# Performance work log

Hardware: AMD Instinct MI355X
Metric: run time of the kernel (lower is better)

## Reference

```python
import jax, jax.numpy as jnp
import numpy as np

N_NODES, N_EDGES = 8, 8
NODE_FEAT, EDGE_FEAT = 4, 3
NODE_EMB, EDGE_EMB = 9, 8
N_LAYER = 3
N_QUBITS = NODE_EMB + EDGE_EMB + 2  # 19

H_GATE = (jnp.array([[1, 1], [1, -1]], jnp.complex64) / np.sqrt(2).astype(np.float32))
CNOT4 = jnp.asarray(np.array([[1, 0, 0, 0], [0, 1, 0, 0], [0, 0, 0, 1], [0, 0, 1, 0]],
                             np.complex64).reshape(2, 2, 2, 2))


def rx_mat(t):
    c = jnp.cos(0.5 * t).astype(jnp.complex64)
    s = (-1j) * jnp.sin(0.5 * t).astype(jnp.complex64)
    return jnp.stack([jnp.stack([c, s]), jnp.stack([s, c])])


def rz_mat(t):
    e = jnp.exp(-0.5j * t.astype(jnp.complex64))
    z = jnp.zeros((), jnp.complex64)
    return jnp.stack([jnp.stack([e, z]), jnp.stack([z, jnp.conj(e)])])


def apply_1q(psi, U, w):
    psi = jnp.tensordot(U, psi, axes=((1,), (w,)))
    return jnp.moveaxis(psi, 0, w)


def apply_cnot(psi, c, t):
    psi = jnp.tensordot(CNOT4, psi, axes=((2, 3), (c, t)))
    return jnp.moveaxis(psi, (0, 1), (c, t))


def gcn_conv(x, src, dst, W, b, n):
    # PyG GCNConv: add self-loops, symmetric D^-1/2 (A+I) D^-1/2 normalization
    h = x @ W  # (n, out)
    src2 = jnp.concatenate([src, jnp.arange(n)])
    dst2 = jnp.concatenate([dst, jnp.arange(n)])
    deg = jax.ops.segment_sum(jnp.ones(src2.shape[0], x.dtype), dst2, num_segments=n)
    dis = jnp.where(deg > 0, jax.lax.rsqrt(jnp.maximum(deg, 1e-12)), 0.0)
    coef = dis[src2] * dis[dst2]
    out = jax.ops.segment_sum(h[src2] * coef[:, None], dst2, num_segments=n)
    return out + b


def quantum_circuit(feats, qweights):
    psi = jnp.zeros((2,) * N_QUBITS, jnp.complex64).at[(0,) * N_QUBITS].set(1.0)
    # feature_map: Hadamards + BasicEntanglerLayers(1 layer, rotation=RZ)
    for q in range(N_QUBITS):
        psi = apply_1q(psi, H_GATE, q)
    for q in range(N_QUBITS):
        psi = apply_1q(psi, rz_mat(feats[q]), q)
    for q in range(N_QUBITS):
        psi = apply_cnot(psi, q, (q + 1) % N_QUBITS)
    # two ansatz blocks (weights first dim is 2), each with N_LAYER layers
    for i in range(2):
        w = qweights[i]  # (N_QUBITS, N_LAYER)
        for j in range(N_LAYER):
            for q in range(N_QUBITS):
                psi = apply_1q(psi, rx_mat(w[q, j]), q)
                psi = apply_1q(psi, rz_mat(w[q, j]), q)
            for q in range(N_QUBITS):
                psi = apply_cnot(psi, q, (q + 1) % N_QUBITS)
    pr = jnp.sum(jnp.abs(psi.reshape(2, -1)) ** 2, axis=1)  # marginal of qubit 0
    return (pr[0] - pr[1]).astype(jnp.float32)  # <Z_0>


def setup_inputs() -> dict:
    key = jax.random.key(0)
    ks = jax.random.split(key, 20)
    inp = {
        "edge_index": jax.random.randint(ks[0], (2, N_EDGES), 0, N_NODES),
        "state": jax.random.normal(ks[1], (N_NODES, NODE_FEAT), jnp.float32),
        "mass": jax.random.normal(ks[2], (N_EDGES,), jnp.float32),
        "spin": jax.random.normal(ks[3], (N_EDGES,), jnp.float32),
        "charge": jax.random.normal(ks[4], (N_EDGES,), jnp.float32),
        "p_norm": jax.random.normal(ks[5], (1,), jnp.float32),
        "theta": jax.random.normal(ks[6], (1,), jnp.float32),
        "scattering": jax.random.normal(ks[7], (1,), jnp.float32),
        "gcn_node_w": jax.random.normal(ks[8], (NODE_FEAT, 1), jnp.float32) * 0.3,
        "gcn_node_b": jnp.zeros((1,), jnp.float32),
        "gcn_edge_w": jax.random.normal(ks[9], (EDGE_FEAT, 1), jnp.float32) * 0.3,
        "gcn_edge_b": jnp.zeros((1,), jnp.float32),
        "node_w": jax.random.normal(ks[10], (N_NODES, NODE_EMB), jnp.float32) * 0.3,
        "node_b": jnp.zeros((NODE_EMB,), jnp.float32),
        "edge_w": jax.random.normal(ks[11], (N_EDGES, EDGE_EMB), jnp.float32) * 0.3,
        "edge_b": jnp.zeros((EDGE_EMB,), jnp.float32),
        "qweights": jax.random.normal(ks[12], (2, N_QUBITS, N_LAYER), jnp.float32) * 0.1,
    }
    return inp


def reference(edge_index, state, mass, spin, charge, p_norm, theta, scattering,
              gcn_node_w, gcn_node_b, gcn_edge_w, gcn_edge_b,
              node_w, node_b, edge_w, edge_b, qweights):
    src, dst = edge_index[0], edge_index[1]
    x_edges = jnp.stack([mass, spin, charge], axis=1)  # (E, 3)
    x1 = gcn_conv(state, src, dst, gcn_node_w, gcn_node_b, N_NODES).reshape(-1)
    x1 = x1 @ node_w + node_b  # (NODE_EMB,)
    x2 = gcn_conv(x_edges, src, dst, gcn_edge_w, gcn_edge_b, N_EDGES).reshape(-1)
    x2 = x2 @ edge_w + edge_b  # (EDGE_EMB,)
    feats = jnp.concatenate([x1, x2, p_norm.reshape(-1), theta.reshape(-1)])  # (N_QUBITS,)
    return quantum_circuit(feats, qweights)
```

## Files before the change

kernel.cpp:

```cpp
#include <hip/hip_runtime.h>

#define NQ 19
#define SZ (1u << NQ)

__global__ __launch_bounds__(128)
void k_prep(const int* __restrict__ ei, const float* __restrict__ state,
            const float* __restrict__ mass, const float* __restrict__ spin,
            const float* __restrict__ charge, const float* __restrict__ p_norm,
            const float* __restrict__ theta,
            const float* __restrict__ gnw, const float* __restrict__ gnb,
            const float* __restrict__ gew, const float* __restrict__ geb,
            const float* __restrict__ nw, const float* __restrict__ nb,
            const float* __restrict__ ew, const float* __restrict__ eb,
            const float* __restrict__ qw,
            float2* __restrict__ G, float2* __restrict__ E0,
            float2* __restrict__ E1)
{
    __shared__ double feats[NQ];
    int tid = threadIdx.x;
    if (tid == 0) {
        double deg[8], dis[8], h[8], o1[8], he[8], o2[8];
        for (int v = 0; v < 8; ++v) deg[v] = 1.0;
        for (int e = 0; e < 8; ++e) deg[ei[8 + e]] += 1.0;
        for (int v = 0; v < 8; ++v) dis[v] = 1.0 / sqrt(deg[v]);
        for (int v = 0; v < 8; ++v) {
            double s = 0.0;
            for (int k = 0; k < 4; ++k) s += (double)state[v * 4 + k] * (double)gnw[k];
            h[v] = s;
        }
        for (int v = 0; v < 8; ++v) o1[v] = h[v] * dis[v] * dis[v] + (double)gnb[0];
        for (int e = 0; e < 8; ++e) {
            int s = ei[e], d = ei[8 + e];
            o1[d] += h[s] * dis[s] * dis[d];
        }
        for (int j = 0; j < 9; ++j) {
            double a = (double)nb[j];
            for (int v = 0; v < 8; ++v) a += o1[v] * (double)nw[v * 9 + j];
            feats[j] = a;
        }
        for (int e = 0; e < 8; ++e)
            he[e] = (double)mass[e] * (double)gew[0] + (double)spin[e] * (double)gew[1]
                  + (double)charge[e] * (double)gew[2];
        for (int v = 0; v < 8; ++v) o2[v] = he[v] * dis[v] * dis[v] + (double)geb[0];
        for (int e = 0; e < 8; ++e) {
            int s = ei[e], d = ei[8 + e];
            o2[d] += he[s] * dis[s] * dis[d];
        }
        for (int j = 0; j < 8; ++j) {
            double a = (double)eb[j];
            for (int v = 0; v < 8; ++v) a += o2[v] * (double)ew[v * 8 + j];
            feats[9 + j] = a;
        }
        feats[17] = (double)p_norm[0];
        feats[18] = (double)theta[0];
    }
    __syncthreads();
    for (int g = tid; g < 6 * NQ; g += blockDim.x) {
        int l = g / NQ, q = g % NQ;
        int i = l / 3, j = l % 3;
        double t = (double)qw[i * (NQ * 3) + q * 3 + j];
        double c = cos(0.5 * t), s = sin(0.5 * t);
        int k = 18 - q;
        float2* Ug = &G[(l * NQ + k) * 4];
        Ug[0] = make_float2((float)(c * c), (float)(-s * c));
        Ug[1] = make_float2((float)(-s * s), (float)(-c * s));
        Ug[2] = make_float2((float)(s * s), (float)(-c * s));
        Ug[3] = make_float2((float)(c * c), (float)(s * c));
    }
    double S = 0.0;
    for (int q = 0; q < NQ; ++q) S += feats[q];
    for (int m = tid; m < 1024; m += blockDim.x) {
        double a = -0.5 * S;
        for (int k = 0; k < 10; ++k)
            if ((m >> k) & 1) a += feats[18 - k];
        double sp, cp;
        sincos(a, &sp, &cp);
        E0[m] = make_float2((float)cp, (float)sp);
    }
    const double amp = 1.0 / sqrt((double)SZ);
    for (int m = tid; m < 512; m += blockDim.x) {
        double a = 0.0;
        for (int k = 0; k < 9; ++k)
            if ((m >> k) & 1) a += feats[8 - k];
        double sp, cp;
        sincos(a, &sp, &cp);
        E1[m] = make_float2((float)(amp * cp), (float)(amp * sp));
    }
}

__device__ __forceinline__ unsigned pinv(unsigned c)
{
    unsigned y = (c ^ (c >> 1)) & 0x1FFFFu;
    unsigned c0 = c & 1u, c17 = (c >> 17) & 1u, c18 = (c >> 18) & 1u;
    return y | ((c0 ^ c17 ^ c18) << 17) | ((c0 ^ c18) << 18);
}

__device__ __forceinline__ void butterfly(float2& a, float2& b,
                                          float2 u00, float2 u01,
                                          float2 u10, float2 u11)
{
    float2 na, nb;
    na.x = u00.x * a.x - u00.y * a.y + u01.x * b.x - u01.y * b.y;
    na.y = u00.x * a.y + u00.y * a.x + u01.x * b.y + u01.y * b.x;
    nb.x = u10.x * a.x - u10.y * a.y + u11.x * b.x - u11.y * b.y;
    nb.y = u10.x * a.y + u10.y * a.x + u11.x * b.y + u11.y * b.x;
    a = na;
    b = nb;
}

__global__ __launch_bounds__(512)
void k_layerA(const float2* __restrict__ in, float2* __restrict__ out,
              const float2* __restrict__ G, int layer,
              const float2* __restrict__ E0, const float2* __restrict__ E1,
              int first)
{
    __shared__ float2 sh[2048];
    unsigned base = blockIdx.x << 11;
    if (first) {
        for (unsigned l = threadIdx.x; l < 2048u; l += 512u) {
            unsigned b = pinv(base | l);
            float2 e0 = E0[b & 1023u], e1 = E1[b >> 10];
            sh[l] = make_float2(e0.x * e1.x - e0.y * e1.y,
                                e0.x * e1.y + e0.y * e1.x);
        }
    } else {
        for (unsigned l = threadIdx.x; l < 2048u; l += 512u)
            sh[l] = in[pinv(base | l)];
    }
    __syncthreads();
    const float2* Gl = G + layer * NQ * 4;
    for (int bit = 0; bit <= 10; ++bit) {
        float2 u00 = Gl[bit * 4 + 0], u01 = Gl[bit * 4 + 1];
        float2 u10 = Gl[bit * 4 + 2], u11 = Gl[bit * 4 + 3];
        unsigned m = 1u << bit;
        for (unsigned p = threadIdx.x; p < 1024u; p += 512u) {
            unsigned l0 = ((p >> bit) << (bit + 1)) | (p & (m - 1u));
            unsigned l1 = l0 | m;
            float2 a = sh[l0], b = sh[l1];
            butterfly(a, b, u00, u01, u10, u11);
            sh[l0] = a;
            sh[l1] = b;
        }
        __syncthreads();
    }
    for (unsigned l = threadIdx.x; l < 2048u; l += 512u)
        out[base | l] = sh[l];
}

__global__ __launch_bounds__(512)
void k_layerB(float2* __restrict__ buf, const float2* __restrict__ G, int layer,
              int do_reduce, double* __restrict__ partial)
{
    __shared__ float2 sh[2048];
    unsigned blk = blockIdx.x;
    for (unsigned l = threadIdx.x; l < 2048u; l += 512u) {
        unsigned idx = ((l >> 3) << 11) | (blk << 3) | (l & 7u);
        sh[l] = buf[idx];
    }
    __syncthreads();
    const float2* Gl = G + layer * NQ * 4;
    for (int bit = 11; bit <= 18; ++bit) {
        float2 u00 = Gl[bit * 4 + 0], u01 = Gl[bit * 4 + 1];
        float2 u10 = Gl[bit * 4 + 2], u11 = Gl[bit * 4 + 3];
        int lb = bit - 8;
        unsigned m = 1u << lb;
        for (unsigned p = threadIdx.x; p < 1024u; p += 512u) {
            unsigned l0 = ((p >> lb) << (lb + 1)) | (p & (m - 1u));
            unsigned l1 = l0 | m;
            float2 a = sh[l0], b = sh[l1];
            butterfly(a, b, u00, u01, u10, u11);
            sh[l0] = a;
            sh[l1] = b;
        }
        __syncthreads();
    }
    if (do_reduce) {
        __shared__ double sm[512];
        double acc = 0.0;
        for (unsigned l = threadIdx.x; l < 2048u; l += 512u) {
            unsigned idx = ((l >> 3) << 11) | (blk << 3) | (l & 7u);
            float2 v = sh[l];
            double w = (double)v.x * v.x + (double)v.y * v.y;
            acc += (__popc(idx & 0x3FFFFu) & 1) ? -w : w;
        }
        sm[threadIdx.x] = acc;
        __syncthreads();
        for (int st = 256; st > 0; st >>= 1) {
            if ((int)threadIdx.x < st) sm[threadIdx.x] += sm[threadIdx.x + st];
            __syncthreads();
        }
        if (threadIdx.x == 0) partial[blk] = sm[0];
    } else {
        for (unsigned l = threadIdx.x; l < 2048u; l += 512u) {
            unsigned idx = ((l >> 3) << 11) | (blk << 3) | (l & 7u);
            buf[idx] = sh[l];
        }
    }
}

__global__ __launch_bounds__(256)
void k_final(const double* __restrict__ partial, float* __restrict__ out)
{
    __shared__ double sm[256];
    sm[threadIdx.x] = partial[threadIdx.x];
    __syncthreads();
    for (int st = 128; st > 0; st >>= 1) {
        if ((int)threadIdx.x < st) sm[threadIdx.x] += sm[threadIdx.x + st];
        __syncthreads();
    }
    if (threadIdx.x == 0) out[0] = (float)sm[0];
}

extern "C" void kernel_launch(void* const* d_in, const int* in_sizes, int n_in,
                              void* d_out, int out_size, void* d_ws, size_t ws_size,
                              hipStream_t stream)
{
    const int*   ei      = (const int*)d_in[0];
    const float* state   = (const float*)d_in[1];
    const float* mass    = (const float*)d_in[2];
    const float* spin    = (const float*)d_in[3];
    const float* charge  = (const float*)d_in[4];
    const float* p_norm  = (const float*)d_in[5];
    const float* theta   = (const float*)d_in[6];
    const float* gnw     = (const float*)d_in[8];
    const float* gnb     = (const float*)d_in[9];
    const float* gew     = (const float*)d_in[10];
    const float* geb     = (const float*)d_in[11];
    const float* nw      = (const float*)d_in[12];
    const float* nb      = (const float*)d_in[13];
    const float* ew      = (const float*)d_in[14];
    const float* eb      = (const float*)d_in[15];
    const float* qw      = (const float*)d_in[16];

    char* ws = (char*)d_ws;
    float2* G       = (float2*)(ws);
    float2* E0      = (float2*)(ws + 4096);
    float2* E1      = (float2*)(ws + 12288);
    double* partial = (double*)(ws + 16384);
    float2* buf0    = (float2*)(ws + 32768);
    float2* buf1    = buf0 + SZ;

    k_prep<<<1, 128, 0, stream>>>(ei, state, mass, spin, charge, p_norm, theta,
                                  gnw, gnb, gew, geb, nw, nb, ew, eb, qw,
                                  G, E0, E1);

    float2* bufs[2] = {buf0, buf1};
    for (int l = 0; l < 6; ++l) {
        float2* in  = bufs[l & 1];
        float2* out = bufs[(l & 1) ^ 1];
        k_layerA<<<256, 512, 0, stream>>>(in, out, G, l, E0, E1, l == 0);
        k_layerB<<<256, 512, 0, stream>>>(out, G, l, l == 5, partial);
    }
    k_final<<<1, 256, 0, stream>>>(partial, (float*)d_out);
}
```

Baseline: 123.3 us.

## Apply gates in registers, 3 qubits per pass, with padded LDS transposes

Each thread now keeps 8 amplitudes in registers and applies three single-qubit gates per pass. Between passes it exchanges data through padded, double-buffered LDS tiles, which replaces 11 and 8 per-bit shared-memory passes with about 4 and 3 passes. This cuts LDS traffic and __syncthreads barriers, and global loads and stores use float4 where the layout allows. Block size drops to 256 threads, so fewer threads are available to hide latency, and the index remapping is more complex.

```diff
diff --git a/kernel.cpp b/kernel.cpp
--- a/kernel.cpp
+++ b/kernel.cpp
@@ -95,9 +95,11 @@
     return y | ((c0 ^ c17 ^ c18) << 17) | ((c0 ^ c18) << 18);
 }
 
-__device__ __forceinline__ void butterfly(float2& a, float2& b,
-                                          float2 u00, float2 u01,
-                                          float2 u10, float2 u11)
+__device__ __forceinline__ unsigned padl(unsigned l) { return l + 2u * (l >> 3); }
+
+__device__ __forceinline__ void bfly(float2& a, float2& b,
+                                     float2 u00, float2 u01,
+                                     float2 u10, float2 u11)
 {
     float2 na, nb;
     na.x = u00.x * a.x - u00.y * a.y + u01.x * b.x - u01.y * b.y;
@@ -108,92 +110,159 @@
     b = nb;
 }
 
-__global__ __launch_bounds__(512)
+__device__ __forceinline__ void apply_gates(float2 r[8], const float2* __restrict__ Gl,
+                                            int ampbit0, int jbit0, int n)
+{
+    #pragma unroll
+    for (int k = 0; k < n; ++k) {
+        const float2 u00 = Gl[(ampbit0 + k) * 4 + 0];
+        const float2 u01 = Gl[(ampbit0 + k) * 4 + 1];
+        const float2 u10 = Gl[(ampbit0 + k) * 4 + 2];
+        const float2 u11 = Gl[(ampbit0 + k) * 4 + 3];
+        const int m = 1 << (jbit0 + k);
+        #pragma unroll
+        for (int j = 0; j < 8; ++j)
+            if (!(j & m)) bfly(r[j], r[j | m], u00, u01, u10, u11);
+    }
+}
+
+__global__ __launch_bounds__(256)
 void k_layerA(const float2* __restrict__ in, float2* __restrict__ out,
               const float2* __restrict__ G, int layer,
               const float2* __restrict__ E0, const float2* __restrict__ E1,
               int first)
 {
-    __shared__ float2 sh[2048];
-    unsigned base = blockIdx.x << 11;
+    __shared__ __align__(16) float2 lds0[2560];
+    __shared__ __align__(16) float2 lds1[2560];
+    const unsigned t = threadIdx.x;
+    const unsigned base = blockIdx.x << 11;
+    const float2* Gl = G + layer * NQ * 4;
+    float2 r[8];
+
     if (first) {
-        for (unsigned l = threadIdx.x; l < 2048u; l += 512u) {
-            unsigned b = pinv(base | l);
+        #pragma unroll
+        for (int j = 0; j < 8; ++j) {
+            unsigned b = pinv(base | (t * 8u + (unsigned)j));
             float2 e0 = E0[b & 1023u], e1 = E1[b >> 10];
-            sh[l] = make_float2(e0.x * e1.x - e0.y * e1.y,
-                                e0.x * e1.y + e0.y * e1.x);
+            r[j] = make_float2(e0.x * e1.x - e0.y * e1.y,
+                               e0.x * e1.y + e0.y * e1.x);
         }
     } else {
-        for (unsigned l = threadIdx.x; l < 2048u; l += 512u)
-            sh[l] = in[pinv(base | l)];
-    }
-    __syncthreads();
-    const float2* Gl = G + layer * NQ * 4;
-    for (int bit = 0; bit <= 10; ++bit) {
-        float2 u00 = Gl[bit * 4 + 0], u01 = Gl[bit * 4 + 1];
-        float2 u10 = Gl[bit * 4 + 2], u11 = Gl[bit * 4 + 3];
-        unsigned m = 1u << bit;
-        for (unsigned p = threadIdx.x; p < 1024u; p += 512u) {
-            unsigned l0 = ((p >> bit) << (bit + 1)) | (p & (m - 1u));
-            unsigned l1 = l0 | m;
-            float2 a = sh[l0], b = sh[l1];
-            butterfly(a, b, u00, u01, u10, u11);
-            sh[l0] = a;
-            sh[l1] = b;
-        }
-        __syncthreads();
-    }
-    for (unsigned l = threadIdx.x; l < 2048u; l += 512u)
-        out[base | l] = sh[l];
-}
-
-__global__ __launch_bounds__(512)
+        #pragma unroll
+        for (int j = 0; j < 8; ++j)
+            r[j] = in[pinv(base | (t * 8u + (unsigned)j))];
+    }
+    apply_gates(r, Gl, 0, 0, 3);
+
+    #pragma unroll
+    for (int jh = 0; jh < 4; ++jh) {
+        unsigned l = t * 8u + (unsigned)jh * 2u;
+        *reinterpret_cast<float4*>(&lds0[padl(l)]) =
+            make_float4(r[2 * jh].x, r[2 * jh].y, r[2 * jh + 1].x, r[2 * jh + 1].y);
+    }
+    __syncthreads();
+    #pragma unroll
+    for (int j = 0; j < 8; ++j)
+        r[j] = lds0[padl((t & 7u) | ((unsigned)j << 3) | ((t >> 3) << 6))];
+    apply_gates(r, Gl, 3, 0, 3);
+
+    #pragma unroll
+    for (int j = 0; j < 8; ++j)
+        lds1[padl((t & 7u) | ((unsigned)j << 3) | ((t >> 3) << 6))] = r[j];
+    __syncthreads();
+    #pragma unroll
+    for (int j = 0; j < 8; ++j)
+        r[j] = lds1[padl((t & 63u) | ((unsigned)j << 6) | ((t >> 6) << 9))];
+    apply_gates(r, Gl, 6, 0, 3);
+
+    #pragma unroll
+    for (int j = 0; j < 8; ++j)
+        lds0[padl((t & 63u) | ((unsigned)j << 6) | ((t >> 6) << 9))] = r[j];
+    __syncthreads();
+    #pragma unroll
+    for (int jh = 0; jh < 4; ++jh) {
+        float4 v = *reinterpret_cast<const float4*>(
+            &lds0[padl((t << 1) | ((unsigned)jh << 9))]);
+        r[2 * jh]     = make_float2(v.x, v.y);
+        r[2 * jh + 1] = make_float2(v.z, v.w);
+    }
+    apply_gates(r, Gl, 9, 1, 2);
+
+    #pragma unroll
+    for (int jh = 0; jh < 4; ++jh) {
+        unsigned l = (t << 1) | ((unsigned)jh << 9);
+        *reinterpret_cast<float4*>(&out[base | l]) =
+            make_float4(r[2 * jh].x, r[2 * jh].y, r[2 * jh + 1].x, r[2 * jh + 1].y);
+    }
+}
+
+__global__ __launch_bounds__(256)
 void k_layerB(float2* __restrict__ buf, const float2* __restrict__ G, int layer,
               int do_reduce, double* __restrict__ partial)
 {
-    __shared__ float2 sh[2048];
-    unsigned blk = blockIdx.x;
-    for (unsigned l = threadIdx.x; l < 2048u; l += 512u) {
-        unsigned idx = ((l >> 3) << 11) | (blk << 3) | (l & 7u);
-        sh[l] = buf[idx];
-    }
-    __syncthreads();
+    __shared__ __align__(16) float2 lds0[2560];
+    __shared__ __align__(16) float2 lds1[2560];
+    const unsigned t = threadIdx.x;
+    const unsigned blk = blockIdx.x;
     const float2* Gl = G + layer * NQ * 4;
-    for (int bit = 11; bit <= 18; ++bit) {
-        float2 u00 = Gl[bit * 4 + 0], u01 = Gl[bit * 4 + 1];
-        float2 u10 = Gl[bit * 4 + 2], u11 = Gl[bit * 4 + 3];
-        int lb = bit - 8;
-        unsigned m = 1u << lb;
-        for (unsigned p = threadIdx.x; p < 1024u; p += 512u) {
-            unsigned l0 = ((p >> lb) << (lb + 1)) | (p & (m - 1u));
-            unsigned l1 = l0 | m;
-            float2 a = sh[l0], b = sh[l1];
-            butterfly(a, b, u00, u01, u10, u11);
-            sh[l0] = a;
-            sh[l1] = b;
-        }
+    float2 r[8];
+
+    #pragma unroll
+    for (int j = 0; j < 8; ++j) {
+        unsigned g = (blk << 3) | (t & 7u) | ((unsigned)j << 11) | ((t >> 3) << 14);
+        r[j] = buf[g];
+    }
+    apply_gates(r, Gl, 11, 0, 3);
+
+    #pragma unroll
+    for (int j = 0; j < 8; ++j)
+        lds0[padl((t & 7u) | ((unsigned)j << 3) | ((t >> 3) << 6))] = r[j];
+    __syncthreads();
+    #pragma unroll
+    for (int j = 0; j < 8; ++j)
+        r[j] = lds0[padl((t & 63u) | ((unsigned)j << 6) | ((t >> 6) << 9))];
+    apply_gates(r, Gl, 14, 0, 3);
+
+    #pragma unroll
+    for (int j = 0; j < 8; ++j)
+        lds1[padl((t & 63u) | ((unsigned)j << 6) | ((t >> 6) << 9))] = r[j];
+    __syncthreads();
+    #pragma unroll
+    for (int jh = 0; jh < 4; ++jh) {
+        float4 v = *reinterpret_cast<const float4*>(
+            &lds1[padl((t << 1) | ((unsigned)jh << 9))]);
+        r[2 * jh]     = make_float2(v.x, v.y);
+        r[2 * jh + 1] = make_float2(v.z, v.w);
+    }
+    apply_gates(r, Gl, 17, 1, 2);
+
+    if (do_reduce) {
+        __shared__ double sm[256];
+        double acc = 0.0;
+        #pragma unroll
+        for (int jh = 0; jh < 4; ++jh) {
+            unsigned l0 = (t << 1) | ((unsigned)jh << 9);
+            unsigned g0 = (blk << 3) | (l0 & 7u) | ((l0 >> 3) << 11);
+            float2 a = r[2 * jh], b = r[2 * jh + 1];
+            double w0 = (double)a.x * a.x + (double)a.y * a.y;
+            double w1 = (double)b.x * b.x + (double)b.y * b.y;
+            double d = w0 - w1;
+            acc += (__popc(g0 & 0x3FFFFu) & 1) ? -d : d;
+        }
+        sm[t] = acc;
         __syncthreads();
-    }
-    if (do_reduce) {
-        __shared__ double sm[512];
-        double acc = 0.0;
-        for (unsigned l = threadIdx.x; l < 2048u; l += 512u) {
-            unsigned idx = ((l >> 3) << 11) | (blk << 3) | (l & 7u);
-            float2 v = sh[l];
-            double w = (double)v.x * v.x + (double)v.y * v.y;
-            acc += (__popc(idx & 0x3FFFFu) & 1) ? -w : w;
-        }
-        sm[threadIdx.x] = acc;
-        __syncthreads();
-        for (int st = 256; st > 0; st >>= 1) {
-            if ((int)threadIdx.x < st) sm[threadIdx.x] += sm[threadIdx.x + st];
+        for (int st = 128; st > 0; st >>= 1) {
+            if ((int)t < st) sm[t] += sm[t + st];
             __syncthreads();
         }
-        if (threadIdx.x == 0) partial[blk] = sm[0];
+        if (t == 0) partial[blk] = sm[0];
     } else {
-        for (unsigned l = threadIdx.x; l < 2048u; l += 512u) {
-            unsigned idx = ((l >> 3) << 11) | (blk << 3) | (l & 7u);
-            buf[idx] = sh[l];
+        #pragma unroll
+        for (int jh = 0; jh < 4; ++jh) {
+            unsigned l = (t << 1) | ((unsigned)jh << 9);
+            unsigned g = (blk << 3) | (l & 7u) | ((l >> 3) << 11);
+            *reinterpret_cast<float4*>(&buf[g]) =
+                make_float4(r[2 * jh].x, r[2 * jh].y, r[2 * jh + 1].x, r[2 * jh + 1].y);
         }
     }
 }
@@ -248,8 +317,8 @@
     for (int l = 0; l < 6; ++l) {
         float2* in  = bufs[l & 1];
         float2* out = bufs[(l & 1) ^ 1];
-        k_layerA<<<256, 512, 0, stream>>>(in, out, G, l, E0, E1, l == 0);
-        k_layerB<<<256, 512, 0, stream>>>(out, G, l, l == 5, partial);
+        k_layerA<<<256, 256, 0, stream>>>(in, out, G, l, E0, E1, l == 0);
+        k_layerB<<<256, 256, 0, stream>>>(out, G, l, l == 5, partial);
     }
     k_final<<<1, 256, 0, stream>>>(partial, (float*)d_out);
 }
```

Measured after the change: 98.99 us. -19.7%, faster.
